# Kernel optimization log

Hardware: AMD Instinct MI355X
Metric: run time of the kernel (lower is better)

## Reference

```python
import jax, jax.numpy as jnp
import numpy as np

N, E, G = 100000, 1600000, 1024
BN_EPS = 1e-5
NEG_SLOPE = 0.2


def setup_inputs() -> dict:
    key = jax.random.key(0)
    ks = jax.random.split(key, 8)
    x = jax.random.normal(ks[0], (N, 128), dtype=jnp.float32)
    edge_index = jax.random.randint(ks[1], (2, E), 0, N, dtype=jnp.int64)
    batch = jnp.sort(jax.random.randint(ks[2], (N,), 0, G, dtype=jnp.int64))
    Wl = jax.random.normal(ks[3], (3, 128, 128), dtype=jnp.float32) * 0.08
    bl = jnp.zeros((3, 128), dtype=jnp.float32)
    Wr = jax.random.normal(ks[4], (3, 128, 128), dtype=jnp.float32) * 0.08
    bn_gamma = jnp.ones((3, 128), dtype=jnp.float32)
    bn_beta = jnp.zeros((3, 128), dtype=jnp.float32)
    bn2_gamma = jnp.ones((128,), dtype=jnp.float32)
    bn2_beta = jnp.zeros((128,), dtype=jnp.float32)
    fc_W = jax.random.normal(ks[5], (128, 64), dtype=jnp.float32) * 0.08
    fc_b = jnp.zeros((64,), dtype=jnp.float32)
    return {"x": x, "edge_index": edge_index, "batch": batch, "Wl": Wl, "bl": bl,
            "Wr": Wr, "bn_gamma": bn_gamma, "bn_beta": bn_beta,
            "bn2_gamma": bn2_gamma, "bn2_beta": bn2_beta, "fc_W": fc_W, "fc_b": fc_b}


def _batch_norm(h, gamma, beta):
    # training-mode BatchNorm1d: batch statistics, biased variance
    mu = jnp.mean(h, axis=0)
    var = jnp.mean((h - mu) ** 2, axis=0)
    return gamma * (h - mu) * jax.lax.rsqrt(var + BN_EPS) + beta


def reference(x, edge_index, batch, Wl, bl, Wr, bn_gamma, bn_beta,
              bn2_gamma, bn2_beta, fc_W, fc_b):
    src, dst = edge_index[0], edge_index[1]
    # in-degree of each destination node (for mean aggregation)
    deg = jax.ops.segment_sum(jnp.ones((E,), dtype=x.dtype), dst, num_segments=N)
    inv_deg = jnp.where(deg > 0, 1.0 / jnp.maximum(deg, 1.0), 0.0)[:, None]  # [N,1]
    h = x
    for i in range(3):
        # SAGEConv: out = lin_l(mean_{j in N(i)} h_j) + lin_r(h_i)
        agg = jax.ops.segment_sum(h[src], dst, num_segments=N) * inv_deg  # [N,H]
        h = agg @ Wl[i] + bl[i] + h @ Wr[i]
        h = jax.nn.leaky_relu(_batch_norm(h, bn_gamma[i], bn_beta[i]), NEG_SLOPE)
        # dropout omitted (eval-mode / deterministic reference)
    pooled = jax.ops.segment_sum(h, batch, num_segments=G)  # [G,H] global_add_pool
    out = _batch_norm(pooled, bn2_gamma, bn2_beta) @ fc_W + fc_b  # [G,latent]
    return out
```

## Files before the change

kernel.cpp:

```cpp
#include <hip/hip_runtime.h>

#define HD 128
#define NCOPY 32
#define BSH 8
#define BSZ 256
#define EPB 4096

typedef __attribute__((ext_vector_type(8))) short short8;
typedef __attribute__((ext_vector_type(4))) float f32x4;

union ABu { unsigned long long u[2]; short8 s8; };

typedef const __attribute__((address_space(1))) void* gas_t;
typedef __attribute__((address_space(3))) void* las_t;

__device__ inline float bf2f(ushort u) {
    union { unsigned int i; float f; } x; x.i = ((unsigned int)u) << 16; return x.f;
}
__device__ inline float bflo(unsigned int u) {
    union { unsigned int i; float f; } x; x.i = u << 16; return x.f;
}
__device__ inline float bfhi(unsigned int u) {
    union { unsigned int i; float f; } x; x.i = u & 0xffff0000u; return x.f;
}
__device__ inline ushort f2bf(float f) {
    union { float f; unsigned int i; } x; x.f = f;
    unsigned int r = x.i + 0x7FFF + ((x.i >> 16) & 1);
    return (ushort)(r >> 16);
}

__device__ inline short8 frag_read(const ushort* tile, int row, int kk, int kg) {
    const char* rowp = (const char*)(tile + row * 64);
    int sw = (row & 7) << 4;
    int b0 = kk * 64 + kg * 8;
    int a0 = (b0 & 15) | ((b0 & ~15) ^ sw);
    int b1 = b0 + 32;
    int a1 = (b1 & 15) | ((b1 & ~15) ^ sw);
    ABu u;
    u.u[0] = *(const unsigned long long*)(rowp + a0);
    u.u[1] = *(const unsigned long long*)(rowp + a1);
    return u.s8;
}

__global__ __launch_bounds__(256) void k_prepcount(
        const float* __restrict__ x, ushort* __restrict__ xb, int total4,
        const float* __restrict__ Wl, const float* __restrict__ Wr,
        ushort* __restrict__ WTS, int wtTotal,
        const int* __restrict__ dst, int* __restrict__ bucketCount, int E, int NB, int nPB) {
    __shared__ int hist[512];
    if (blockIdx.x < nPB) {
        for (int i = threadIdx.x; i < NB; i += 256) hist[i] = 0;
        __syncthreads();
        int e0 = blockIdx.x * EPB;
#pragma unroll
        for (int j = 0; j < 16; ++j) {
            int e = e0 + j * 256 + threadIdx.x;
            if (e < E) atomicAdd(&hist[dst[e] >> BSH], 1);
        }
        __syncthreads();
        for (int i = threadIdx.x; i < NB; i += 256)
            if (hist[i]) atomicAdd(&bucketCount[i], hist[i]);
    } else {
        int i = (blockIdx.x - nPB) * 256 + threadIdx.x;
        int stride = (gridDim.x - nPB) * 256;
        for (int idx = i; idx < total4; idx += stride) {
            float4 v = ((const float4*)x)[idx];
            ushort4 o;
            o.x = f2bf(v.x); o.y = f2bf(v.y); o.z = f2bf(v.z); o.w = f2bf(v.w);
            ((ushort4*)xb)[idx] = o;
        }
        for (int idx = i; idx < wtTotal; idx += stride) {
            int l = idx >> 15;
            int r = idx & 32767;
            int c = r >> 13;
            int r2 = r & 8191;
            int col = r2 >> 6;
            int kin = r2 & 63;
            int sb = kin >> 3, j = kin & 7;
            int b = sb ^ (col & 7);
            int k = c * 64 + b * 8 + j;
            float v = (k < 128) ? Wl[l * 16384 + k * 128 + col]
                                : Wr[l * 16384 + (k - 128) * 128 + col];
            WTS[idx] = f2bf(v);
        }
    }
}

__global__ __launch_bounds__(256) void kp_part(const int* __restrict__ src,
                                               const int* __restrict__ dst,
                                               const int* __restrict__ bCount,
                                               int* __restrict__ gCursor,
                                               unsigned int* __restrict__ packed,
                                               int E, int NB) {
    __shared__ int bbase[512];
    __shared__ int pair[256];
    __shared__ int hist[512], lbase[512], lcur[512];
    int tid = threadIdx.x;
    int i0 = 2 * tid, i1 = 2 * tid + 1;
    int v0 = (i0 < NB) ? bCount[i0] : 0;
    int v1 = (i1 < NB) ? bCount[i1] : 0;
    pair[tid] = v0 + v1;
    __syncthreads();
    for (int off = 1; off < 256; off <<= 1) {
        int t = 0;
        if (tid >= off) t = pair[tid - off];
        __syncthreads();
        if (tid >= off) pair[tid] += t;
        __syncthreads();
    }
    int incl = pair[tid];
    bbase[i0] = incl - v0 - v1;
    bbase[i1] = incl - v1;
    for (int i = tid; i < NB; i += 256) hist[i] = 0;
    __syncthreads();

    int e0 = blockIdx.x * EPB;
    int b[16]; unsigned int w[16];
#pragma unroll
    for (int j = 0; j < 16; ++j) {
        int e = e0 + j * 256 + tid;
        b[j] = -1;
        if (e < E) {
            int d = dst[e];
            int s = src[e];
            b[j] = d >> BSH;
            w[j] = (unsigned int)s | (((unsigned int)d & (BSZ - 1)) << 17);
            atomicAdd(&hist[b[j]], 1);
        }
    }
    __syncthreads();
    for (int i = tid; i < NB; i += 256) {
        int c = hist[i];
        lbase[i] = c ? (bbase[i] + atomicAdd(&gCursor[i], c)) : 0;
        lcur[i] = 0;
    }
    __syncthreads();
#pragma unroll
    for (int j = 0; j < 16; ++j) {
        if (b[j] >= 0) {
            int r = atomicAdd(&lcur[b[j]], 1);
            packed[lbase[b[j]] + r] = w[j];
        }
    }
}

__global__ __launch_bounds__(256) void kp_degfill(const unsigned int* __restrict__ packed,
                                                  const int* __restrict__ bCount,
                                                  int* __restrict__ rowptr,
                                                  float* __restrict__ inv,
                                                  int* __restrict__ csr, int N, int E, int NB) {
    __shared__ int dcnt[BSZ];
    __shared__ int scn[BSZ];
    __shared__ int rp[BSZ];
    __shared__ int red[256];
    int bkt = blockIdx.x;
    int tid = threadIdx.x;
    int n0 = bkt << BSH;
    int partial = 0;
    for (int i = tid; i < bkt; i += 256) partial += bCount[i];
    red[tid] = partial;
    __syncthreads();
    for (int off = 128; off > 0; off >>= 1) {
        if (tid < off) red[tid] += red[tid + off];
        __syncthreads();
    }
    int beg = red[0];
    int end = beg + bCount[bkt];
    __syncthreads();
    dcnt[tid] = 0;
    __syncthreads();
    for (int e = beg + tid; e < end; e += 256)
        atomicAdd(&dcnt[packed[e] >> 17], 1);
    __syncthreads();
    int v = dcnt[tid];
    scn[tid] = v;
    __syncthreads();
    for (int off = 1; off < 256; off <<= 1) {
        int t = 0;
        if (tid >= off) t = scn[tid - off];
        __syncthreads();
        if (tid >= off) scn[tid] += t;
        __syncthreads();
    }
    int rpv = beg + scn[tid] - v;
    int n = n0 + tid;
    if (n < N) {
        rowptr[n] = rpv;
        inv[n] = (v > 0) ? (1.0f / (float)v) : 0.0f;
    }
    if (bkt == 0 && tid == 0) rowptr[N] = E;
    __syncthreads();
    dcnt[tid] = 0;
    rp[tid] = rpv;
    __syncthreads();
    for (int e = beg + tid; e < end; e += 256) {
        unsigned int wv = packed[e];
        int ld = wv >> 17;
        int p = atomicAdd(&dcnt[ld], 1);
        csr[rp[ld] + p] = (int)(wv & 0x1FFFF);
    }
}

__global__ __launch_bounds__(256) void k_agg(const ushort* __restrict__ h,
                                             const int* __restrict__ rowptr,
                                             const int* __restrict__ csr,
                                             const float* __restrict__ inv,
                                             ushort* __restrict__ agg, int N) {
    int node = blockIdx.x * 4 + (threadIdx.x >> 6);
    if (node >= N) return;
    int lane = threadIdx.x & 63;
    int g = lane >> 4, ln = lane & 15;
    int beg = rowptr[node], end = rowptr[node + 1];
    float a[8], b[8];
#pragma unroll
    for (int j = 0; j < 8; ++j) { a[j] = 0.f; b[j] = 0.f; }
    for (int e = beg + g; e < end; e += 8) {
        int s0 = csr[e];
        uint4 v0 = *(const uint4*)&h[(size_t)s0 * HD + ln * 8];
        int e1 = e + 4;
        if (e1 < end) {
            int s1 = csr[e1];
            uint4 v1 = *(const uint4*)&h[(size_t)s1 * HD + ln * 8];
            b[0] += bflo(v1.x); b[1] += bfhi(v1.x);
            b[2] += bflo(v1.y); b[3] += bfhi(v1.y);
            b[4] += bflo(v1.z); b[5] += bfhi(v1.z);
            b[6] += bflo(v1.w); b[7] += bfhi(v1.w);
        }
        a[0] += bflo(v0.x); a[1] += bfhi(v0.x);
        a[2] += bflo(v0.y); a[3] += bfhi(v0.y);
        a[4] += bflo(v0.z); a[5] += bfhi(v0.z);
        a[6] += bflo(v0.w); a[7] += bfhi(v0.w);
    }
#pragma unroll
    for (int j = 0; j < 8; ++j) {
        a[j] += b[j];
        a[j] += __shfl_xor(a[j], 16);
        a[j] += __shfl_xor(a[j], 32);
    }
    if (lane < 16) {
        float iv = inv[node];
        ushort o[8];
#pragma unroll
        for (int j = 0; j < 8; ++j) o[j] = f2bf(a[j] * iv);
        *(uint4*)&agg[(size_t)node * HD + ln * 8] = *(uint4*)o;
    }
}

__global__ __launch_bounds__(256) void k_gemm(
        const ushort* __restrict__ X1, const ushort* __restrict__ X2,
        const ushort* __restrict__ WTS, const float* __restrict__ bias,
        ushort* __restrict__ out, float* __restrict__ stats, int N) {
    __shared__ ushort As[128 * 64];
    __shared__ ushort Bs[128 * 64];
    int tid = threadIdx.x;
    int lane = tid & 63, wid = tid >> 6;
    int wr = wid >> 1, wc = wid & 1;
    int ln15 = lane & 15, kg = lane >> 4;
    int rbase = blockIdx.x * 128;
    int lrow = lane >> 3;
    int sb = lane & 7;

    f32x4 acc[4][4];
#pragma unroll
    for (int m = 0; m < 4; ++m)
#pragma unroll
        for (int nn = 0; nn < 4; ++nn) acc[m][nn] = (f32x4){0.f, 0.f, 0.f, 0.f};

    for (int c = 0; c < 4; ++c) {
        const ushort* X = (c < 2) ? X1 : X2;
        size_t cbyte = (size_t)(c & 1) * 128;
        const char* bsrc = (const char*)WTS + (size_t)c * 16384;
#pragma unroll
        for (int p = 0; p < 4; ++p) {
            int instr = wid * 4 + p;
            int row_local = instr * 8 + lrow;
            int grow = rbase + row_local;
            if (grow >= N) grow = N - 1;
            const char* gpA = (const char*)X + (size_t)grow * 256 + cbyte
                              + (((sb ^ (row_local & 7)) << 4));
            __builtin_amdgcn_global_load_lds((gas_t)gpA,
                    (las_t)((char*)As + instr * 1024), 16, 0, 0);
            const char* gpB = bsrc + instr * 1024 + lane * 16;
            __builtin_amdgcn_global_load_lds((gas_t)gpB,
                    (las_t)((char*)Bs + instr * 1024), 16, 0, 0);
        }
        __syncthreads();
#pragma unroll
        for (int kk = 0; kk < 2; ++kk) {
            short8 af[4], bfr[4];
#pragma unroll
            for (int m = 0; m < 4; ++m)
                af[m] = frag_read(As, wr * 64 + m * 16 + ln15, kk, kg);
#pragma unroll
            for (int nn = 0; nn < 4; ++nn)
                bfr[nn] = frag_read(Bs, wc * 64 + nn * 16 + ln15, kk, kg);
#pragma unroll
            for (int m = 0; m < 4; ++m)
#pragma unroll
                for (int nn = 0; nn < 4; ++nn)
                    acc[m][nn] = __builtin_amdgcn_mfma_f32_16x16x32_bf16(af[m], bfr[nn], acc[m][nn], 0, 0, 0);
        }
        __syncthreads();
    }

    float s[4] = {0.f, 0.f, 0.f, 0.f};
    float q[4] = {0.f, 0.f, 0.f, 0.f};
    float bv[4];
#pragma unroll
    for (int nn = 0; nn < 4; ++nn) bv[nn] = bias[wc * 64 + nn * 16 + ln15];
#pragma unroll
    for (int m = 0; m < 4; ++m) {
#pragma unroll
        for (int j = 0; j < 4; ++j) {
            int row = rbase + wr * 64 + m * 16 + kg * 4 + j;
            if (row < N) {
#pragma unroll
                for (int nn = 0; nn < 4; ++nn) {
                    float v = acc[m][nn][j] + bv[nn];
                    out[(size_t)row * HD + wc * 64 + nn * 16 + ln15] = f2bf(v);
                    s[nn] += v; q[nn] += v * v;
                }
            }
        }
    }
#pragma unroll
    for (int nn = 0; nn < 4; ++nn) {
        s[nn] += __shfl_xor(s[nn], 16); s[nn] += __shfl_xor(s[nn], 32);
        q[nn] += __shfl_xor(q[nn], 16); q[nn] += __shfl_xor(q[nn], 32);
    }
    if (lane < 16) {
        int slot = (blockIdx.x & (NCOPY - 1)) * 256;
#pragma unroll
        for (int nn = 0; nn < 4; ++nn) {
            int col = wc * 64 + nn * 16 + lane;
            atomicAdd(&stats[slot + col], s[nn]);
            atomicAdd(&stats[slot + 128 + col], q[nn]);
        }
    }
}

__global__ __launch_bounds__(256) void k_apply(ushort* buf, const float* __restrict__ stats,
                                               const float* __restrict__ gamma,
                                               const float* __restrict__ beta,
                                               float count, int total8) {
    __shared__ float sc[HD], sh[HD];
    int tid = threadIdx.x;
    if (tid < HD) {
        float s = 0.f, q = 0.f;
        for (int i = 0; i < NCOPY; ++i) { s += stats[i * 256 + tid]; q += stats[i * 256 + 128 + tid]; }
        float mean = s / count;
        float var = fmaxf(q / count - mean * mean, 0.f);
        float scale = gamma[tid] * rsqrtf(var + 1e-5f);
        sc[tid] = scale;
        sh[tid] = beta[tid] - mean * scale;
    }
    __syncthreads();
    int i = blockIdx.x * blockDim.x + tid;
    int stride = gridDim.x * blockDim.x;
    for (int idx = i; idx < total8; idx += stride) {
        int cb = (idx * 8) & (HD - 1);
        uint4 v = ((const uint4*)buf)[idx];
        float f[8];
        f[0] = bflo(v.x); f[1] = bfhi(v.x);
        f[2] = bflo(v.y); f[3] = bfhi(v.y);
        f[4] = bflo(v.z); f[5] = bfhi(v.z);
        f[6] = bflo(v.w); f[7] = bfhi(v.w);
        ushort o[8];
#pragma unroll
        for (int j = 0; j < 8; ++j) {
            float y = f[j] * sc[cb + j] + sh[cb + j];
            y = (y > 0.f) ? y : 0.2f * y;
            o[j] = f2bf(y);
        }
        ((uint4*)buf)[idx] = *(uint4*)o;
    }
}

__global__ void k_poolapply(const ushort* __restrict__ h, const float* __restrict__ stats,
                            const float* __restrict__ gamma, const float* __restrict__ beta,
                            float count, const int* __restrict__ batch,
                            float* __restrict__ pooled, int N) {
    int c = threadIdx.x;
    float s = 0.f, q = 0.f;
    for (int i = 0; i < NCOPY; ++i) { s += stats[i * 256 + c]; q += stats[i * 256 + 128 + c]; }
    float mean = s / count;
    float var = fmaxf(q / count - mean * mean, 0.f);
    float sc = gamma[c] * rsqrtf(var + 1e-5f);
    float sh = beta[c] - mean * sc;
    int n0 = blockIdx.x * 64;
    if (n0 >= N) return;
    int nend = min(n0 + 64, N);
    float acc = 0.f;
    int cur = batch[n0];
    for (int n = n0; n < nend; ++n) {
        int b = batch[n];
        if (b != cur) { atomicAdd(&pooled[cur * HD + c], acc); acc = 0.f; cur = b; }
        float y = bf2f(h[(size_t)n * HD + c]) * sc + sh;
        y = (y > 0.f) ? y : 0.2f * y;
        acc += y;
    }
    atomicAdd(&pooled[cur * HD + c], acc);
}

__global__ void k_colstats(const float* __restrict__ X, float* __restrict__ stats, int rows) {
    int c = threadIdx.x;
    float s = 0.f, q = 0.f;
    for (int r = blockIdx.x; r < rows; r += gridDim.x) {
        float v = X[r * HD + c];
        s += v; q += v * v;
    }
    int slot = (blockIdx.x & (NCOPY - 1)) * 256;
    atomicAdd(&stats[slot + c], s);
    atomicAdd(&stats[slot + 128 + c], q);
}

__global__ void k_final(const float* __restrict__ pooled, const float* __restrict__ stats2,
                        const float* __restrict__ bn2g, const float* __restrict__ bn2b,
                        const float* __restrict__ fcW, const float* __restrict__ fcb,
                        float* __restrict__ outp, float countG) {
    __shared__ float Wlds[HD * 64];
    __shared__ float prow[HD];
    int tid = threadIdx.x;
    for (int i = tid; i < HD * 64 / 4; i += 128) ((float4*)Wlds)[i] = ((const float4*)fcW)[i];
    float s = 0.f, q = 0.f;
    for (int i = 0; i < NCOPY; ++i) { s += stats2[i * 256 + tid]; q += stats2[i * 256 + 128 + tid]; }
    float mean = s / countG;
    float var = fmaxf(q / countG - mean * mean, 0.f);
    float scale = bn2g[tid] * rsqrtf(var + 1e-5f);
    float shift = bn2b[tid] - mean * scale;
    int g = blockIdx.x;
    prow[tid] = pooled[g * HD + tid] * scale + shift;
    __syncthreads();
    if (tid < 64) {
        float acc = fcb[tid];
#pragma unroll 8
        for (int c = 0; c < HD; ++c) acc += prow[c] * Wlds[c * 64 + tid];
        outp[g * 64 + tid] = acc;
    }
}

extern "C" void kernel_launch(void* const* d_in, const int* in_sizes, int n_in,
                              void* d_out, int out_size, void* d_ws, size_t ws_size,
                              hipStream_t stream) {
    const float* x     = (const float*)d_in[0];
    const int*   ei    = (const int*)d_in[1];
    const int*   batch = (const int*)d_in[2];
    const float* Wl    = (const float*)d_in[3];
    const float* bl    = (const float*)d_in[4];
    const float* Wr    = (const float*)d_in[5];
    const float* bng   = (const float*)d_in[6];
    const float* bnb   = (const float*)d_in[7];
    const float* bn2g  = (const float*)d_in[8];
    const float* bn2b  = (const float*)d_in[9];
    const float* fcW   = (const float*)d_in[10];
    const float* fcb   = (const float*)d_in[11];

    int N = in_sizes[0] / HD;
    int E = in_sizes[1] / 2;
    int G = out_size / 64;
    const int* src = ei;
    const int* dst = ei + E;

    char* p = (char*)d_ws;
    auto alloc = [&](size_t bytes) -> void* {
        void* r = (void*)p;
        p += (bytes + 255) & ~(size_t)255;
        return r;
    };
    int NB = (N + BSZ - 1) >> BSH;
    int nPB = (E + EPB - 1) / EPB;

    int*    rowptr   = (int*)alloc((size_t)(N + 1) * 4);
    int*    csr      = (int*)alloc((size_t)E * 4);
    float*  inv      = (float*)alloc((size_t)N * 4);
    ushort* WTS      = (ushort*)alloc((size_t)3 * 128 * 256 * 2);
    ushort* xb       = (ushort*)alloc((size_t)N * HD * 2);
    ushort* aggb     = (ushort*)alloc((size_t)N * HD * 2);
    ushort* hb1      = (ushort*)alloc((size_t)N * HD * 2);
    ushort* hb2      = (ushort*)alloc((size_t)N * HD * 2);
    char*   zbase    = (char*)alloc(0);
    float*  statsAll = (float*)alloc((size_t)4 * NCOPY * 256 * 4);
    float*  pooled   = (float*)alloc((size_t)G * HD * 4);
    int*    bCount   = (int*)alloc((size_t)NB * 4);
    int*    gCursor  = (int*)alloc((size_t)NB * 4);
    size_t  zbytes   = (size_t)((char*)p - zbase);

    float* stats0  = statsAll;
    float* stats1  = statsAll + NCOPY * 256;
    float* statsL2 = statsAll + 2 * NCOPY * 256;
    float* stats2  = statsAll + 3 * NCOPY * 256;

    unsigned int* packed = (unsigned int*)aggb;

    float* outp = (float*)d_out;
    int total4 = N * HD / 4;
    int total8 = N * HD / 8;
    int ggrid = (N + 127) / 128;
    int agrid = (N + 3) / 4;
    float fN = (float)N, fG = (float)G;

    hipMemsetAsync(zbase, 0, zbytes, stream);
    k_prepcount<<<nPB + 1024, 256, 0, stream>>>(x, xb, total4, Wl, Wr, WTS, 3 * 128 * 256,
                                                dst, bCount, E, NB, nPB);
    kp_part<<<nPB, 256, 0, stream>>>(src, dst, bCount, gCursor, packed, E, NB);
    kp_degfill<<<NB, 256, 0, stream>>>(packed, bCount, rowptr, inv, csr, N, E, NB);

    k_agg<<<agrid, 256, 0, stream>>>(xb, rowptr, csr, inv, aggb, N);
    k_gemm<<<ggrid, 256, 0, stream>>>(aggb, xb, WTS, bl, hb1, stats0, N);
    k_apply<<<2048, 256, 0, stream>>>(hb1, stats0, bng, bnb, fN, total8);

    k_agg<<<agrid, 256, 0, stream>>>(hb1, rowptr, csr, inv, aggb, N);
    k_gemm<<<ggrid, 256, 0, stream>>>(aggb, hb1, WTS + 32768, bl + 128, hb2, stats1, N);
    k_apply<<<2048, 256, 0, stream>>>(hb2, stats1, bng + 128, bnb + 128, fN, total8);

    k_agg<<<agrid, 256, 0, stream>>>(hb2, rowptr, csr, inv, aggb, N);
    k_gemm<<<ggrid, 256, 0, stream>>>(aggb, hb2, WTS + 65536, bl + 256, hb1, statsL2, N);
    k_poolapply<<<(N + 63) / 64, HD, 0, stream>>>(hb1, statsL2, bng + 256, bnb + 256, fN,
                                                  batch, pooled, N);

    k_colstats<<<64, HD, 0, stream>>>(pooled, stats2, G);
    k_final<<<G, HD, 0, stream>>>(pooled, stats2, bn2g, bn2b, fcW, fcb, outp, fG);
}
```

Baseline: 381.5 us.

## Load GEMM weight fragments directly from global in MFMA layout, shrink memset

Reorders the bf16 weight matrix at prep time into the per-lane MFMA fragment layout so the GEMM kernel reads B fragments straight from global memory into registers, dropping the B tile from shared memory and its LDS reads. Halving LDS use may allow more resident blocks per CU. It also moves zeroing of the stats and pooled buffers into the prep kernel so the memset covers only the small bucket counters. Weight reads now go through cache per block instead of LDS, which could add some global load latency.

```diff
diff --git a/kernel.cpp b/kernel.cpp
--- a/kernel.cpp
+++ b/kernel.cpp
@@ -46,6 +46,7 @@
         const float* __restrict__ x, ushort* __restrict__ xb, int total4,
         const float* __restrict__ Wl, const float* __restrict__ Wr,
         ushort* __restrict__ WTS, int wtTotal,
+        float* __restrict__ zbuf, int ztotal4,
         const int* __restrict__ dst, int* __restrict__ bucketCount, int E, int NB, int nPB) {
     __shared__ int hist[512];
     if (blockIdx.x < nPB) {
@@ -72,17 +73,19 @@
         for (int idx = i; idx < wtTotal; idx += stride) {
             int l = idx >> 15;
             int r = idx & 32767;
-            int c = r >> 13;
-            int r2 = r & 8191;
-            int col = r2 >> 6;
-            int kin = r2 & 63;
-            int sb = kin >> 3, j = kin & 7;
-            int b = sb ^ (col & 7);
-            int k = c * 64 + b * 8 + j;
+            int ckk = r >> 12;
+            int c = ckk >> 1, kk = ckk & 1;
+            int r2 = r & 4095;
+            int col = r2 >> 5;
+            int r3 = r2 & 31;
+            int kg = r3 >> 3, e = r3 & 7;
+            int k = c * 64 + kk * 32 + kg * 4 + (e & 3) + ((e >> 2) << 4);
             float v = (k < 128) ? Wl[l * 16384 + k * 128 + col]
                                 : Wr[l * 16384 + (k - 128) * 128 + col];
             WTS[idx] = f2bf(v);
         }
+        float4 z = make_float4(0.f, 0.f, 0.f, 0.f);
+        for (int idx = i; idx < ztotal4; idx += stride) ((float4*)zbuf)[idx] = z;
     }
 }
 
@@ -251,7 +254,6 @@
         const ushort* __restrict__ WTS, const float* __restrict__ bias,
         ushort* __restrict__ out, float* __restrict__ stats, int N) {
     __shared__ ushort As[128 * 64];
-    __shared__ ushort Bs[128 * 64];
     int tid = threadIdx.x;
     int lane = tid & 63, wid = tid >> 6;
     int wr = wid >> 1, wc = wid & 1;
@@ -269,7 +271,6 @@
     for (int c = 0; c < 4; ++c) {
         const ushort* X = (c < 2) ? X1 : X2;
         size_t cbyte = (size_t)(c & 1) * 128;
-        const char* bsrc = (const char*)WTS + (size_t)c * 16384;
 #pragma unroll
         for (int p = 0; p < 4; ++p) {
             int instr = wid * 4 + p;
@@ -277,28 +278,30 @@
             int grow = rbase + row_local;
             if (grow >= N) grow = N - 1;
             const char* gpA = (const char*)X + (size_t)grow * 256 + cbyte
-                              + (((sb ^ (row_local & 7)) << 4));
+                              + ((sb ^ (row_local & 7)) << 4);
             __builtin_amdgcn_global_load_lds((gas_t)gpA,
                     (las_t)((char*)As + instr * 1024), 16, 0, 0);
-            const char* gpB = bsrc + instr * 1024 + lane * 16;
-            __builtin_amdgcn_global_load_lds((gas_t)gpB,
-                    (las_t)((char*)Bs + instr * 1024), 16, 0, 0);
-        }
+        }
+        short8 bfr[2][4];
+#pragma unroll
+        for (int kk = 0; kk < 2; ++kk)
+#pragma unroll
+            for (int nn = 0; nn < 4; ++nn) {
+                int col = wc * 64 + nn * 16 + ln15;
+                bfr[kk][nn] = *(const short8*)&WTS[((size_t)(c * 2 + kk) * 128 + col) * 32 + kg * 8];
+            }
         __syncthreads();
 #pragma unroll
         for (int kk = 0; kk < 2; ++kk) {
-            short8 af[4], bfr[4];
+            short8 af[4];
 #pragma unroll
             for (int m = 0; m < 4; ++m)
                 af[m] = frag_read(As, wr * 64 + m * 16 + ln15, kk, kg);
 #pragma unroll
-            for (int nn = 0; nn < 4; ++nn)
-                bfr[nn] = frag_read(Bs, wc * 64 + nn * 16 + ln15, kk, kg);
-#pragma unroll
             for (int m = 0; m < 4; ++m)
 #pragma unroll
                 for (int nn = 0; nn < 4; ++nn)
-                    acc[m][nn] = __builtin_amdgcn_mfma_f32_16x16x32_bf16(af[m], bfr[nn], acc[m][nn], 0, 0, 0);
+                    acc[m][nn] = __builtin_amdgcn_mfma_f32_16x16x32_bf16(af[m], bfr[kk][nn], acc[m][nn], 0, 0, 0);
         }
         __syncthreads();
     }
@@ -478,9 +481,9 @@
     ushort* aggb     = (ushort*)alloc((size_t)N * HD * 2);
     ushort* hb1      = (ushort*)alloc((size_t)N * HD * 2);
     ushort* hb2      = (ushort*)alloc((size_t)N * HD * 2);
-    char*   zbase    = (char*)alloc(0);
     float*  statsAll = (float*)alloc((size_t)4 * NCOPY * 256 * 4);
     float*  pooled   = (float*)alloc((size_t)G * HD * 4);
+    char*   zbase    = (char*)alloc(0);
     int*    bCount   = (int*)alloc((size_t)NB * 4);
     int*    gCursor  = (int*)alloc((size_t)NB * 4);
     size_t  zbytes   = (size_t)((char*)p - zbase);
@@ -489,6 +492,7 @@
     float* stats1  = statsAll + NCOPY * 256;
     float* statsL2 = statsAll + 2 * NCOPY * 256;
     float* stats2  = statsAll + 3 * NCOPY * 256;
+    int ztotal4 = (4 * NCOPY * 256 * 4 + G * HD * 4) / 16;
 
     unsigned int* packed = (unsigned int*)aggb;
 
@@ -501,6 +505,7 @@
 
     hipMemsetAsync(zbase, 0, zbytes, stream);
     k_prepcount<<<nPB + 1024, 256, 0, stream>>>(x, xb, total4, Wl, Wr, WTS, 3 * 128 * 256,
+                                                statsAll, ztotal4,
                                                 dst, bCount, E, NB, nPB);
     kp_part<<<nPB, 256, 0, stream>>>(src, dst, bCount, gCursor, packed, E, NB);
     kp_degfill<<<NB, 256, 0, stream>>>(packed, bCount, rowptr, inv, csr, N, E, NB);
```

New measurement: 378.0 us. No clear change (-0.9%).
